# Kernel optimization log

Measured on AMD Instinct MI355X. Metric: run time of the kernel, lower is better.

Reference implementation:

```python
import jax, jax.numpy as jnp
import numpy as np

# Model dims (match init_kwargs / input_specs)
B, CIN, COUT = 32, 32, 64
H, W = 128, 128
KH, KW = 3, 3
MAXCN = 64                    # max entries in connect_nums_list
HO, WO = H - KH + 1, W - KW + 1   # padding=0, stride=1


def setup_inputs() -> dict:
    key = jax.random.key(0)
    k1, k2, k3, k4 = jax.random.split(key, 4)
    x = jax.random.normal(k1, (B, CIN, H, W), dtype=jnp.float32)
    # padded kernel bank: [out_channel, connection_slot, kh, kw]
    weights = jax.random.normal(k2, (COUT, MAXCN, KH, KW), dtype=jnp.float32)
    # per-pixel bias map per output channel (original inits zeros; random exercises it)
    bias = jax.random.normal(k3, (COUT, HO, WO), dtype=jnp.float32) * 0.1
    connect_nums = jax.random.randint(k4, (COUT,), 1, MAXCN + 1, dtype=jnp.int32)
    return {"x": x, "weights": weights, "bias": bias, "connect_nums": connect_nums}


def reference(x, weights, bias, connect_nums):
    O, J = weights.shape[0], weights.shape[1]
    # mask out kernel slots beyond each channel's connection count
    mask = (jnp.arange(J)[None, :] < connect_nums[:, None]).astype(weights.dtype)  # [O,J]
    # slot j reads input channel j % CIN; conv is linear, so fold duplicate-channel
    # kernels into one effective dense kernel [O, CIN, KH, KW]
    onehot = jax.nn.one_hot(jnp.arange(J) % CIN, CIN, dtype=weights.dtype)  # [J,C]
    kdense = jnp.einsum('ojhw,oj,jc->ochw', weights, mask, onehot)
    out = jax.lax.conv_general_dilated(
        x, kdense, window_strides=(1, 1), padding='VALID',
        dimension_numbers=('NCHW', 'OIHW', 'NCHW'))  # [B,O,HO,WO]
    return out + bias[None]
```

## Files before the change

kernel.cpp:

```cpp
#include <hip/hip_runtime.h>

#define B_    32
#define CIN   32
#define COUT  64
#define H_    128
#define W_    128
#define HO_   126
#define WO_   126
#define MAXCN 64

typedef __attribute__((ext_vector_type(8))) short short8;
typedef __attribute__((ext_vector_type(4))) float floatx4;

static __device__ __forceinline__ unsigned short f2bf(float f) {
    union { float f; unsigned u; } v; v.f = f;
    unsigned r = v.u + 0x7fff + ((v.u >> 16) & 1);
    return (unsigned short)(r >> 16);
}

__global__ void fold_bf16(const float* __restrict__ w,
                          const int* __restrict__ cn,
                          unsigned short* __restrict__ wk) {
    int idx = blockIdx.x * 256 + threadIdx.x;
    if (idx >= 9 * COUT * CIN) return;
    int c   = idx & 31;
    int oc  = (idx >> 5) & 63;
    int tap = idx >> 11;
    int n = cn[oc];
    float v = 0.0f;
    if (c < n)      v += w[(oc * MAXCN + c) * 9 + tap];
    if (c + 32 < n) v += w[(oc * MAXCN + c + 32) * 9 + tap];
    wk[idx] = f2bf(v);
}

__global__ __launch_bounds__(256)
void nchw_to_nhwc_bf16(const float* __restrict__ x,
                       unsigned short* __restrict__ xb) {
    const int b = blockIdx.y, y = blockIdx.x;
    const int t = threadIdx.x;
    const int c8  = t & 3;
    const int xi0 = t >> 2;
    const float* xp = x + (size_t)b * CIN * H_ * W_ + (size_t)y * W_;
#pragma unroll
    for (int it = 0; it < 2; ++it) {
        const int xi = xi0 + it * 64;
        __align__(16) unsigned short v[8];
#pragma unroll
        for (int j = 0; j < 8; ++j) {
            const int c = c8 * 8 + j;
            v[j] = f2bf(xp[(size_t)c * (H_ * W_) + xi]);
        }
        *(uint4*)(xb + (((size_t)b * H_ + y) * W_ + xi) * CIN + c8 * 8) =
            *(const uint4*)v;
    }
}

__global__ __launch_bounds__(256)
void conv_mfma(const unsigned short* __restrict__ xb,
               const unsigned short* __restrict__ wk,
               const float* __restrict__ bias,
               float* __restrict__ out) {
    __shared__ __align__(16) unsigned short xs[18 * 18 * 32];
    __shared__ __align__(16) unsigned short ws[9 * 32 * 32];

    const int tile = blockIdx.x;
    const int ocg  = blockIdx.y;
    const int b    = blockIdx.z;
    const int tx = tile & 7, ty = tile >> 3;
    const int x0 = tx * 16, y0 = ty * 16;
    const int tid = threadIdx.x;

    uint4* xs4 = (uint4*)xs;
    for (int idx = tid; idx < 1296; idx += 256) {
        int yy = idx / 72;
        int r  = idx - yy * 72;
        int xc = r >> 2;
        int cp = r & 3;
        int iy = y0 + yy; if (iy > H_ - 1) iy = H_ - 1;
        int ix = x0 + xc; if (ix > W_ - 1) ix = W_ - 1;
        const uint4* s = (const uint4*)(xb + (((size_t)b * H_ + iy) * W_ + ix) * CIN) + cp;
        xs4[idx] = *s;
    }
    uint4* ws4 = (uint4*)ws;
    const uint4* wk4 = (const uint4*)wk;
    for (int idx = tid; idx < 1152; idx += 256) {
        int tap  = idx >> 7;
        int rem  = idx & 127;
        int oc_l = rem >> 2;
        int cp   = rem & 3;
        ws4[idx] = wk4[tap * 256 + (ocg * 32 + oc_l) * 4 + cp];
    }
    __syncthreads();

    const int w_id = tid >> 6;
    const int lane = tid & 63;
    const int quad = lane >> 4, l16 = lane & 15;

    floatx4 acc[4][2];
#pragma unroll
    for (int i = 0; i < 4; ++i)
#pragma unroll
        for (int t = 0; t < 2; ++t) acc[i][t] = (floatx4)0.0f;

#pragma unroll
    for (int kh = 0; kh < 3; ++kh) {
#pragma unroll
        for (int kw = 0; kw < 3; ++kw) {
            const int tap = kh * 3 + kw;
            short8 a[2], bf[4];
#pragma unroll
            for (int t = 0; t < 2; ++t)
                a[t] = *(const short8*)&ws[((tap * 32 + t * 16 + l16) * 32) + quad * 8];
#pragma unroll
            for (int i = 0; i < 4; ++i)
                bf[i] = *(const short8*)&xs[(((4 * w_id + i + kh) * 18 + l16 + kw) * 32) + quad * 8];
#pragma unroll
            for (int i = 0; i < 4; ++i)
#pragma unroll
                for (int t = 0; t < 2; ++t)
                    acc[i][t] = __builtin_amdgcn_mfma_f32_16x16x32_bf16(a[t], bf[i], acc[i][t], 0, 0, 0);
        }
    }

    const int col = x0 + l16;
#pragma unroll
    for (int i = 0; i < 4; ++i) {
        const int y = y0 + 4 * w_id + i;
        if (y >= HO_ || col >= WO_) continue;
#pragma unroll
        for (int t = 0; t < 2; ++t) {
#pragma unroll
            for (int r = 0; r < 4; ++r) {
                const int oc = ocg * 32 + t * 16 + quad * 4 + r;
                out[(((size_t)b * COUT + oc) * HO_ + y) * WO_ + col] =
                    acc[i][t][r] + bias[((size_t)oc * HO_ + y) * WO_ + col];
            }
        }
    }
}

__global__ void fold_kernel(const float* __restrict__ w,
                            const int* __restrict__ cn,
                            float* __restrict__ kd) {
    int idx = blockIdx.x * blockDim.x + threadIdx.x;
    if (idx >= COUT * CIN * 9) return;
    int t = idx % 9;
    int c = (idx / 9) % CIN;
    int o = idx / (9 * CIN);
    int n = cn[o];
    float v = 0.0f;
    if (c < n)      v += w[(o * MAXCN + c) * 9 + t];
    if (c + 32 < n) v += w[(o * MAXCN + c + 32) * 9 + t];
    kd[idx] = v;
}

__global__ __launch_bounds__(256)
void conv_kernel(const float* __restrict__ x,
                 const float* __restrict__ kd,
                 const float* __restrict__ bias,
                 float* __restrict__ out) {
    __shared__ __align__(16) float xsh[CIN * 18 * 20];
    __shared__ __align__(16) float wsh[16 * 289];
    const int b = blockIdx.z, ocg = blockIdx.y, tile = blockIdx.x;
    const int ty = tile >> 3, txx = tile & 7;
    const int y0 = ty * 16, x0 = txx * 16;
    const int tid = threadIdx.x;
    const float* xbp = x + (size_t)b * CIN * H_ * W_;
    for (int idx = tid; idx < CIN * 18 * 18; idx += 256) {
        int c = idx / 324, rem = idx - c * 324, r = rem / 18, col = rem - r * 18;
        int iy = y0 + r;   if (iy > H_ - 1) iy = H_ - 1;
        int ix = x0 + col; if (ix > W_ - 1) ix = W_ - 1;
        xsh[c * 360 + r * 20 + col] = xbp[(c * H_ + iy) * W_ + ix];
    }
    for (int idx = tid; idx < 16 * 288; idx += 256) {
        int oc = idx / 288, rr = idx - oc * 288;
        wsh[oc * 289 + rr] = kd[(ocg * 16 + oc) * 288 + rr];
    }
    __syncthreads();
    const int oc_l = tid & 15, pb = tid >> 4, pby = pb >> 2, pbx = pb & 3;
    float acc[4][4];
#pragma unroll
    for (int i = 0; i < 4; ++i)
#pragma unroll
        for (int j = 0; j < 4; ++j) acc[i][j] = 0.0f;
    const float* xp = &xsh[(pby * 4) * 20 + pbx * 4];
    const float* wp = &wsh[oc_l * 289];
    for (int c = 0; c < CIN; ++c) {
        float xr[6][6];
#pragma unroll
        for (int r = 0; r < 6; ++r) {
            const float* row = xp + c * 360 + r * 20;
            float4 v4 = *reinterpret_cast<const float4*>(row);
            float2 v2 = *reinterpret_cast<const float2*>(row + 4);
            xr[r][0] = v4.x; xr[r][1] = v4.y; xr[r][2] = v4.z;
            xr[r][3] = v4.w; xr[r][4] = v2.x; xr[r][5] = v2.y;
        }
        float wr[9];
#pragma unroll
        for (int t = 0; t < 9; ++t) wr[t] = wp[c * 9 + t];
#pragma unroll
        for (int kh = 0; kh < 3; ++kh)
#pragma unroll
            for (int kw = 0; kw < 3; ++kw) {
                const float wv = wr[kh * 3 + kw];
#pragma unroll
                for (int i = 0; i < 4; ++i)
#pragma unroll
                    for (int j = 0; j < 4; ++j)
                        acc[i][j] = fmaf(xr[i + kh][j + kw], wv, acc[i][j]);
            }
    }
    const int o = ocg * 16 + oc_l;
    const int yb = y0 + pby * 4, xq0 = x0 + pbx * 4;
    float* ob = out + ((size_t)(b * COUT + o)) * HO_ * WO_;
    const float* bb = bias + (size_t)o * HO_ * WO_;
#pragma unroll
    for (int i = 0; i < 4; ++i) {
        int y = yb + i;
        if (y >= HO_) continue;
#pragma unroll
        for (int j = 0; j < 4; ++j) {
            int xq = xq0 + j;
            if (xq >= WO_) continue;
            ob[y * WO_ + xq] = acc[i][j] + bb[y * WO_ + xq];
        }
    }
}

extern "C" void kernel_launch(void* const* d_in, const int* in_sizes, int n_in,
                              void* d_out, int out_size, void* d_ws, size_t ws_size,
                              hipStream_t stream) {
    const float* x    = (const float*)d_in[0];
    const float* w    = (const float*)d_in[1];
    const float* bias = (const float*)d_in[2];
    const int*   cn   = (const int*)d_in[3];
    float* out = (float*)d_out;

    const size_t XB_BYTES = (size_t)B_ * H_ * W_ * CIN * 2;
    const size_t WK_BYTES = (size_t)9 * COUT * CIN * 2;

    if (ws_size >= XB_BYTES + WK_BYTES) {
        unsigned short* xbuf = (unsigned short*)d_ws;
        unsigned short* wkb  = (unsigned short*)((char*)d_ws + XB_BYTES);
        fold_bf16<<<(9 * COUT * CIN + 255) / 256, 256, 0, stream>>>(w, cn, wkb);
        nchw_to_nhwc_bf16<<<dim3(H_, B_), 256, 0, stream>>>(x, xbuf);
        conv_mfma<<<dim3(64, 2, B_), 256, 0, stream>>>(xbuf, wkb, bias, out);
    } else {
        float* kd = (float*)d_ws;
        fold_kernel<<<(COUT * CIN * 9 + 255) / 256, 256, 0, stream>>>(w, cn, kd);
        dim3 grid(64, 4, B_);
        conv_kernel<<<grid, 256, 0, stream>>>(x, kd, bias, out);
    }
}
```

Before: 263.5 us.

## Compute all 64 output channels per block and read input directly from global

Each conv block now covers all 64 output channels instead of 32, which halves the grid and means every input tile is read once rather than twice. The input halo is no longer staged in shared memory. MFMA B-operands are loaded straight from the NHWC bf16 global buffer using precomputed row and column offsets, and the cache is relied on for reuse across taps. Shared memory holds only the full folded weight bank. This raises accumulator registers to 16 floatx4 per thread and adds an occupancy hint in launch bounds. The risks are more global/L1 traffic in the inner loop and register pressure.

```diff
diff --git a/kernel.cpp b/kernel.cpp
--- a/kernel.cpp
+++ b/kernel.cpp
@@ -55,85 +55,82 @@
     }
 }
 
-__global__ __launch_bounds__(256)
+__global__ __launch_bounds__(256, 4)
 void conv_mfma(const unsigned short* __restrict__ xb,
                const unsigned short* __restrict__ wk,
                const float* __restrict__ bias,
                float* __restrict__ out) {
-    __shared__ __align__(16) unsigned short xs[18 * 18 * 32];
-    __shared__ __align__(16) unsigned short ws[9 * 32 * 32];
+    __shared__ __align__(16) unsigned short ws[9 * COUT * CIN];
 
     const int tile = blockIdx.x;
-    const int ocg  = blockIdx.y;
-    const int b    = blockIdx.z;
+    const int b    = blockIdx.y;
     const int tx = tile & 7, ty = tile >> 3;
     const int x0 = tx * 16, y0 = ty * 16;
     const int tid = threadIdx.x;
 
-    uint4* xs4 = (uint4*)xs;
-    for (int idx = tid; idx < 1296; idx += 256) {
-        int yy = idx / 72;
-        int r  = idx - yy * 72;
-        int xc = r >> 2;
-        int cp = r & 3;
-        int iy = y0 + yy; if (iy > H_ - 1) iy = H_ - 1;
-        int ix = x0 + xc; if (ix > W_ - 1) ix = W_ - 1;
-        const uint4* s = (const uint4*)(xb + (((size_t)b * H_ + iy) * W_ + ix) * CIN) + cp;
-        xs4[idx] = *s;
-    }
     uint4* ws4 = (uint4*)ws;
     const uint4* wk4 = (const uint4*)wk;
-    for (int idx = tid; idx < 1152; idx += 256) {
-        int tap  = idx >> 7;
-        int rem  = idx & 127;
-        int oc_l = rem >> 2;
-        int cp   = rem & 3;
-        ws4[idx] = wk4[tap * 256 + (ocg * 32 + oc_l) * 4 + cp];
-    }
+#pragma unroll
+    for (int it = 0; it < 9; ++it) ws4[it * 256 + tid] = wk4[it * 256 + tid];
     __syncthreads();
 
     const int w_id = tid >> 6;
     const int lane = tid & 63;
     const int quad = lane >> 4, l16 = lane & 15;
 
-    floatx4 acc[4][2];
+    int rowoff[6];
+#pragma unroll
+    for (int r = 0; r < 6; ++r) {
+        int iy = y0 + 4 * w_id + r; if (iy > H_ - 1) iy = H_ - 1;
+        rowoff[r] = (b * H_ + iy) * (W_ * CIN);
+    }
+    int coloff[3];
+#pragma unroll
+    for (int kw = 0; kw < 3; ++kw) {
+        int ix = x0 + l16 + kw; if (ix > W_ - 1) ix = W_ - 1;
+        coloff[kw] = ix * CIN + quad * 8;
+    }
+
+    floatx4 acc[4][4];
 #pragma unroll
     for (int i = 0; i < 4; ++i)
 #pragma unroll
-        for (int t = 0; t < 2; ++t) acc[i][t] = (floatx4)0.0f;
+        for (int t = 0; t < 4; ++t) acc[i][t] = (floatx4)0.0f;
 
 #pragma unroll
     for (int kh = 0; kh < 3; ++kh) {
 #pragma unroll
         for (int kw = 0; kw < 3; ++kw) {
             const int tap = kh * 3 + kw;
-            short8 a[2], bf[4];
-#pragma unroll
-            for (int t = 0; t < 2; ++t)
-                a[t] = *(const short8*)&ws[((tap * 32 + t * 16 + l16) * 32) + quad * 8];
+            short8 a[4], bf[4];
+#pragma unroll
+            for (int t = 0; t < 4; ++t)
+                a[t] = *(const short8*)&ws[((tap * COUT + t * 16 + l16) * CIN) + quad * 8];
 #pragma unroll
             for (int i = 0; i < 4; ++i)
-                bf[i] = *(const short8*)&xs[(((4 * w_id + i + kh) * 18 + l16 + kw) * 32) + quad * 8];
+                bf[i] = *(const short8*)(xb + rowoff[i + kh] + coloff[kw]);
 #pragma unroll
             for (int i = 0; i < 4; ++i)
 #pragma unroll
-                for (int t = 0; t < 2; ++t)
+                for (int t = 0; t < 4; ++t)
                     acc[i][t] = __builtin_amdgcn_mfma_f32_16x16x32_bf16(a[t], bf[i], acc[i][t], 0, 0, 0);
         }
     }
 
     const int col = x0 + l16;
-#pragma unroll
-    for (int i = 0; i < 4; ++i) {
-        const int y = y0 + 4 * w_id + i;
-        if (y >= HO_ || col >= WO_) continue;
-#pragma unroll
-        for (int t = 0; t < 2; ++t) {
-#pragma unroll
-            for (int r = 0; r < 4; ++r) {
-                const int oc = ocg * 32 + t * 16 + quad * 4 + r;
-                out[(((size_t)b * COUT + oc) * HO_ + y) * WO_ + col] =
-                    acc[i][t][r] + bias[((size_t)oc * HO_ + y) * WO_ + col];
+    if (col < WO_) {
+#pragma unroll
+        for (int i = 0; i < 4; ++i) {
+            const int y = y0 + 4 * w_id + i;
+            if (y >= HO_) continue;
+#pragma unroll
+            for (int t = 0; t < 4; ++t) {
+#pragma unroll
+                for (int r = 0; r < 4; ++r) {
+                    const int oc = t * 16 + quad * 4 + r;
+                    out[(((size_t)b * COUT + oc) * HO_ + y) * WO_ + col] =
+                        acc[i][t][r] + bias[((size_t)oc * HO_ + y) * WO_ + col];
+                }
             }
         }
     }
@@ -244,7 +241,7 @@
         unsigned short* wkb  = (unsigned short*)((char*)d_ws + XB_BYTES);
         fold_bf16<<<(9 * COUT * CIN + 255) / 256, 256, 0, stream>>>(w, cn, wkb);
         nchw_to_nhwc_bf16<<<dim3(H_, B_), 256, 0, stream>>>(x, xbuf);
-        conv_mfma<<<dim3(64, 2, B_), 256, 0, stream>>>(xbuf, wkb, bias, out);
+        conv_mfma<<<dim3(64, B_), 256, 0, stream>>>(xbuf, wkb, bias, out);
     } else {
         float* kd = (float*)d_ws;
         fold_kernel<<<(COUT * CIN * 9 + 255) / 256, 256, 0, stream>>>(w, cn, kd);
```

Result: slower. 281.8 us (+6.9%).

## Read weights from global in MFMA layout and restripe input tile in LDS

Applied to the files above, without the earlier changes.

The folded bf16 weight layout is changed so that each lane's 8-channel A fragment sits contiguously in global memory, and the conv kernel loads A operands directly from global/L2 instead of staging the weight bank in shared memory. The input tile in LDS is re-laid out as [row][channel-group][x] to change the bank access pattern for the B-fragment reads. LDS use drops and launch bounds now request 6 blocks per CU to raise occupancy. The cost is repeated global weight loads inside the MFMA loop, which may add latency if they miss cache.

```diff
diff --git a/kernel.cpp b/kernel.cpp
--- a/kernel.cpp
+++ b/kernel.cpp
@@ -30,7 +30,7 @@
     float v = 0.0f;
     if (c < n)      v += w[(oc * MAXCN + c) * 9 + tap];
     if (c + 32 < n) v += w[(oc * MAXCN + c + 32) * 9 + tap];
-    wk[idx] = f2bf(v);
+    wk[((tap * 4 + (c >> 3)) * 64 + oc) * 8 + (c & 7)] = f2bf(v);
 }
 
 __global__ __launch_bounds__(256)
@@ -55,13 +55,12 @@
     }
 }
 
-__global__ __launch_bounds__(256)
+__global__ __launch_bounds__(256, 6)
 void conv_mfma(const unsigned short* __restrict__ xb,
                const unsigned short* __restrict__ wk,
                const float* __restrict__ bias,
                float* __restrict__ out) {
-    __shared__ __align__(16) unsigned short xs[18 * 18 * 32];
-    __shared__ __align__(16) unsigned short ws[9 * 32 * 32];
+    __shared__ __align__(16) unsigned short xs[1296 * 8];
 
     const int tile = blockIdx.x;
     const int ocg  = blockIdx.y;
@@ -71,24 +70,27 @@
     const int tid = threadIdx.x;
 
     uint4* xs4 = (uint4*)xs;
-    for (int idx = tid; idx < 1296; idx += 256) {
-        int yy = idx / 72;
-        int r  = idx - yy * 72;
-        int xc = r >> 2;
-        int cp = r & 3;
+    const uint4* xb4 = (const uint4*)(xb + (size_t)b * H_ * W_ * CIN);
+#pragma unroll
+    for (int k = 0; k < 5; ++k) {
+        int idx = k * 256 + tid;
+        int yy  = idx / 72;
+        int rem = idx - yy * 72;
+        int xc  = rem >> 2;
+        int cp  = rem & 3;
         int iy = y0 + yy; if (iy > H_ - 1) iy = H_ - 1;
         int ix = x0 + xc; if (ix > W_ - 1) ix = W_ - 1;
-        const uint4* s = (const uint4*)(xb + (((size_t)b * H_ + iy) * W_ + ix) * CIN) + cp;
-        xs4[idx] = *s;
-    }
-    uint4* ws4 = (uint4*)ws;
-    const uint4* wk4 = (const uint4*)wk;
-    for (int idx = tid; idx < 1152; idx += 256) {
-        int tap  = idx >> 7;
-        int rem  = idx & 127;
-        int oc_l = rem >> 2;
-        int cp   = rem & 3;
-        ws4[idx] = wk4[tap * 256 + (ocg * 32 + oc_l) * 4 + cp];
+        xs4[(yy * 4 + cp) * 18 + xc] = xb4[(iy * W_ + ix) * 4 + cp];
+    }
+    if (tid < 16) {
+        int idx = 1280 + tid;
+        int yy  = idx / 72;
+        int rem = idx - yy * 72;
+        int xc  = rem >> 2;
+        int cp  = rem & 3;
+        int iy = y0 + yy; if (iy > H_ - 1) iy = H_ - 1;
+        int ix = x0 + xc; if (ix > W_ - 1) ix = W_ - 1;
+        xs4[(yy * 4 + cp) * 18 + xc] = xb4[(iy * W_ + ix) * 4 + cp];
     }
     __syncthreads();
 
@@ -96,6 +98,10 @@
     const int lane = tid & 63;
     const int quad = lane >> 4, l16 = lane & 15;
 
+    const short8* wq8 = (const short8*)wk;
+    const int abase = quad * 64 + ocg * 32 + l16;
+    const int bbase = (quad * 18 + l16) * 8;
+
     floatx4 acc[4][2];
 #pragma unroll
     for (int i = 0; i < 4; ++i)
@@ -107,33 +113,34 @@
 #pragma unroll
         for (int kw = 0; kw < 3; ++kw) {
             const int tap = kh * 3 + kw;
-            short8 a[2], bf[4];
-#pragma unroll
-            for (int t = 0; t < 2; ++t)
-                a[t] = *(const short8*)&ws[((tap * 32 + t * 16 + l16) * 32) + quad * 8];
+            short8 a0 = wq8[tap * 256 + abase];
+            short8 a1 = wq8[tap * 256 + abase + 16];
+            short8 bf[4];
 #pragma unroll
             for (int i = 0; i < 4; ++i)
-                bf[i] = *(const short8*)&xs[(((4 * w_id + i + kh) * 18 + l16 + kw) * 32) + quad * 8];
-#pragma unroll
-            for (int i = 0; i < 4; ++i)
-#pragma unroll
-                for (int t = 0; t < 2; ++t)
-                    acc[i][t] = __builtin_amdgcn_mfma_f32_16x16x32_bf16(a[t], bf[i], acc[i][t], 0, 0, 0);
+                bf[i] = *(const short8*)&xs[(4 * w_id + i + kh) * 576 + bbase + kw * 8];
+#pragma unroll
+            for (int i = 0; i < 4; ++i) {
+                acc[i][0] = __builtin_amdgcn_mfma_f32_16x16x32_bf16(a0, bf[i], acc[i][0], 0, 0, 0);
+                acc[i][1] = __builtin_amdgcn_mfma_f32_16x16x32_bf16(a1, bf[i], acc[i][1], 0, 0, 0);
+            }
         }
     }
 
     const int col = x0 + l16;
-#pragma unroll
-    for (int i = 0; i < 4; ++i) {
-        const int y = y0 + 4 * w_id + i;
-        if (y >= HO_ || col >= WO_) continue;
-#pragma unroll
-        for (int t = 0; t < 2; ++t) {
-#pragma unroll
-            for (int r = 0; r < 4; ++r) {
-                const int oc = ocg * 32 + t * 16 + quad * 4 + r;
-                out[(((size_t)b * COUT + oc) * HO_ + y) * WO_ + col] =
-                    acc[i][t][r] + bias[((size_t)oc * HO_ + y) * WO_ + col];
+    if (col < WO_) {
+#pragma unroll
+        for (int i = 0; i < 4; ++i) {
+            const int y = y0 + 4 * w_id + i;
+            if (y >= HO_) continue;
+#pragma unroll
+            for (int t = 0; t < 2; ++t) {
+#pragma unroll
+                for (int r = 0; r < 4; ++r) {
+                    const int oc = ocg * 32 + t * 16 + quad * 4 + r;
+                    out[(((size_t)b * COUT + oc) * HO_ + y) * WO_ + col] =
+                        acc[i][t][r] + bias[((size_t)oc * HO_ + y) * WO_ + col];
+                }
             }
         }
     }
```

New measurement: 298.5 us. 13.3% more time.
